# Kernel tuning notes

Measured on AMD Instinct MI355X. Metric: run time of the kernel, lower is better.

## Reference

```python
import jax, jax.numpy as jnp
import numpy as np

B, N, DIM, H = 16, 1024, 512, 8
HEAD_DIM = DIM // H
SCALE = HEAD_DIM ** -0.5


def _dct_matrix(m):
    # Orthonormal DCT-II matrix, matching cv2.dct: D[0,:]=sqrt(1/m),
    # D[k,n]=sqrt(2/m)*cos(pi*(2n+1)*k/(2m)) for k>0.
    n = jnp.arange(m, dtype=jnp.float32)
    k = n[:, None]
    D = jnp.sqrt(2.0 / m) * jnp.cos(jnp.pi * (2.0 * n[None, :] + 1.0) * k / (2.0 * m))
    return D.at[0, :].set(jnp.sqrt(1.0 / m))


def setup_inputs() -> dict:
    key = jax.random.key(0)
    ks = jax.random.split(key, 9)
    def lin(k, fan_in, shape):
        return jax.random.normal(k, shape, jnp.float32) * (1.0 / np.sqrt(fan_in))
    return {
        "x": jax.random.normal(ks[0], (B, N, DIM), jnp.float32),
        "qkv_w": lin(ks[1], DIM, (DIM, 3 * DIM)),
        "qkv_b": lin(ks[2], DIM, (3 * DIM,)),
        "proj_w": lin(ks[3], DIM, (DIM, DIM)),
        "proj_b": lin(ks[4], DIM, (DIM,)),
        "h1_w": lin(ks[5], DIM, (DIM, DIM // 4)),
        "h1_b": jnp.zeros((DIM // 4,), jnp.float32),
        "h2_w": lin(ks[6], DIM // 4, (DIM // 4, H)),
        "h2_b": jnp.zeros((H,), jnp.float32),
        "freq_w": jnp.float32(0.5),
    }


def _extract_dct_features(x):
    # x: (B, N, C). Mirrors extract_dct_features incl. the .detach() in torch.
    B_, N_, _ = x.shape
    m = int(np.ceil(np.sqrt(N_)))  # static
    x_mean = x.mean(axis=-1)                                   # (B, N)
    A = jnp.pad(x_mean, ((0, 0), (0, m * m - N_))).reshape(B_, m, m)
    D = _dct_matrix(m)
    dct2 = jnp.einsum('km,bmn,ln->bkl', D, A, D)               # 2D DCT per sample
    dct_feat = dct2.reshape(B_, m * m)[:, :N_]
    dct_feat = jnp.clip(dct_feat, -10.0, 10.0)
    norm = jnp.linalg.norm(dct_feat, axis=1, keepdims=True) + 1e-5
    return jax.lax.stop_gradient(dct_feat / norm)              # (B, N)


def reference(x, qkv_w, qkv_b, proj_w, proj_b, h1_w, h1_b, h2_w, h2_b, freq_w):
    B_, N_, C = x.shape
    # QKV projection -> (3, B, H, N, head_dim)
    qkv = (x @ qkv_w + qkv_b).reshape(B_, N_, 3, H, C // H)
    qkv = jnp.transpose(qkv, (2, 0, 3, 1, 4))
    q, k, v = qkv[0] * SCALE, qkv[1], qkv[2]
    attn = jnp.einsum('bhnd,bhmd->bhnm', q, k)                 # (B, H, N, N)

    # Frequency-domain attention term
    dct_feat = _extract_dct_features(x)                        # (B, N)
    x_avg = x.mean(axis=1)                                     # (B, C)
    head_w = jax.nn.relu(x_avg @ h1_w + h1_b) @ h2_w + h2_b    # (B, H)
    weighted = dct_feat[:, None, :] * head_w[:, :, None]       # (B, H, N)
    freq_attn = jnp.einsum('bhn,bhm->bnm', weighted, weighted) # (B, N, N)
    row_sum = jnp.maximum(freq_attn.sum(axis=-1, keepdims=True), 1e-5)
    freq_attn = jnp.clip(freq_attn / row_sum, 0.0, 1.0)

    aw = jax.nn.sigmoid(freq_w)
    attn = (1.0 - aw) * attn + aw * freq_attn[:, None, :, :]
    attn = jax.nn.softmax(attn, axis=-1)

    out = jnp.einsum('bhnm,bhmd->bhnd', attn, v)
    out = jnp.transpose(out, (0, 2, 1, 3)).reshape(B_, N_, C)
    return out @ proj_w + proj_b
```

## Files before the change

kernel.cpp:

```cpp
#include <hip/hip_runtime.h>
#include <hip/hip_bf16.h>
#include <math.h>

#define PI_F  3.14159265358979323846f
#define LOG2E 1.44269504088896340736f

typedef __attribute__((ext_vector_type(8))) short          bf16x8;
typedef __attribute__((ext_vector_type(8))) unsigned short ushort8;
typedef __attribute__((ext_vector_type(4))) float          f32x4;

__device__ __forceinline__ unsigned short f2bf(float f) {
  union { float f; unsigned u; } v; v.f = f;
  unsigned r = v.u + 0x7fffu + ((v.u >> 16) & 1u);
  return (unsigned short)(r >> 16);
}

__device__ __forceinline__ unsigned short f2bf_hw(float f) {
  __hip_bfloat16 h = __float2bfloat16(f);
  return *reinterpret_cast<unsigned short*>(&h);
}

#define GLOAD16(g, l)                                                         \
  __builtin_amdgcn_global_load_lds(                                           \
      (const __attribute__((address_space(1))) void*)(g),                     \
      (__attribute__((address_space(3))) void*)(l), 16, 0, 0)

static const size_t OFF_XB  = 0;
static const size_t OFF_QB  = 16777216;
static const size_t OFF_KB  = 33554432;
static const size_t OFF_VT  = 67108864;
static const size_t OFF_AO  = 83886080;
static const size_t OFF_WT  = 100663296;
static const size_t OFF_PWT = 102236160;
static const size_t OFF_XM  = 102760448;
static const size_t OFF_XA  = 102825984;
static const size_t OFF_DF  = 102858752;
static const size_t OFF_TS  = 102924288;
static const size_t OFF_CR  = 102924352;

__global__ __launch_bounds__(256) void k_xmean_cvt(const float* __restrict__ x,
                                                   float* __restrict__ xmean,
                                                   unsigned short* __restrict__ xb) {
  int row  = blockIdx.x * 4 + (threadIdx.x >> 6);
  int lane = threadIdx.x & 63;
  const float* px = x + (size_t)row * 512 + lane * 8;
  float4 a = ((const float4*)px)[0];
  float4 b = ((const float4*)px)[1];
  ushort8 o;
  o[0] = f2bf(a.x); o[1] = f2bf(a.y); o[2] = f2bf(a.z); o[3] = f2bf(a.w);
  o[4] = f2bf(b.x); o[5] = f2bf(b.y); o[6] = f2bf(b.z); o[7] = f2bf(b.w);
  *(ushort8*)(xb + (size_t)row * 512 + lane * 8) = o;
  float s = a.x + a.y + a.z + a.w + b.x + b.y + b.z + b.w;
  for (int off = 32; off; off >>= 1) s += __shfl_down(s, off);
  if (lane == 0) xmean[row] = s * (1.f / 512.f);
}

__global__ __launch_bounds__(512) void k_xavg(const unsigned short* __restrict__ xb,
                                              float* __restrict__ xavg) {
  int b = blockIdx.x, chunk = blockIdx.y;
  int c = threadIdx.x;
  const unsigned short* px = xb + ((size_t)b * 1024 + (size_t)chunk * 64) * 512 + c;
  float s = 0.f;
#pragma unroll 8
  for (int n = 0; n < 64; ++n) {
    unsigned u = (unsigned)px[(size_t)n * 512] << 16;
    s += *reinterpret_cast<float*>(&u);
  }
  atomicAdd(&xavg[b * 512 + c], s);
}

__global__ __launch_bounds__(1024) void k_dct(const float* __restrict__ xmean,
                                              float* __restrict__ dfeat,
                                              float* __restrict__ tsum) {
  __shared__ float A[32][33], Dm[32][33], Tm[32][33];
  __shared__ float red[1024];
  __shared__ float nrm;
  int b = blockIdx.x, t = threadIdx.x;
  int kk = t >> 5, nn = t & 31;
  A[kk][nn] = xmean[b * 1024 + t];
  float dv = (kk == 0) ? sqrtf(1.f / 32.f)
                       : sqrtf(2.f / 32.f) * cosf(PI_F * (2.f * nn + 1.f) * (float)kk / 64.f);
  Dm[kk][nn] = dv;
  __syncthreads();
  float acc = 0.f;
  for (int m = 0; m < 32; ++m) acc += Dm[kk][m] * A[m][nn];
  Tm[kk][nn] = acc;
  __syncthreads();
  float acc2 = 0.f;
  for (int n = 0; n < 32; ++n) acc2 += Tm[kk][n] * Dm[nn][n];
  float val = fminf(fmaxf(acc2, -10.f), 10.f);
  red[t] = val * val;
  __syncthreads();
  for (int s = 512; s; s >>= 1) { if (t < s) red[t] += red[t + s]; __syncthreads(); }
  if (t == 0) nrm = sqrtf(red[0]) + 1e-5f;
  __syncthreads();
  float dn = val / nrm;
  dfeat[b * 1024 + t] = dn;
  red[t] = dn;
  __syncthreads();
  for (int s = 512; s; s >>= 1) { if (t < s) red[t] += red[t + s]; __syncthreads(); }
  if (t == 0) tsum[b] = red[0];
}

__global__ __launch_bounds__(128) void k_headw(const float* __restrict__ xavg,
                                               const float* __restrict__ h1w,
                                               const float* __restrict__ h1b,
                                               const float* __restrict__ h2w,
                                               const float* __restrict__ h2b,
                                               const float* __restrict__ dfeat,
                                               const float* __restrict__ tsum,
                                               const float* __restrict__ freqw,
                                               float* __restrict__ crow) {
  __shared__ float xa[512];
  __shared__ float h1s[128];
  __shared__ float hw[8];
  int b = blockIdx.x, t = threadIdx.x;
  for (int i = t; i < 512; i += 128) xa[i] = xavg[b * 512 + i] * (1.f / 1024.f);
  __syncthreads();
  float acc = h1b[t];
  for (int c = 0; c < 512; ++c) acc += xa[c] * h1w[c * 128 + t];
  h1s[t] = fmaxf(acc, 0.f);
  __syncthreads();
  if (t < 8) {
    float a2 = h2b[t];
    for (int j = 0; j < 128; ++j) a2 += h1s[j] * h2w[j * 8 + t];
    hw[t] = a2;
  }
  __syncthreads();
  float s = 0.f;
#pragma unroll
  for (int h = 0; h < 8; ++h) s += hw[h] * hw[h];
  float Tb = tsum[b];
  const float aw2 = (1.f / (1.f + __expf(-freqw[0]))) * LOG2E;
  for (int n = t; n < 1024; n += 128) {
    float dn = dfeat[b * 1024 + n];
    float p = s * dn;
    crow[b * 1024 + n] = aw2 * p / fmaxf(p * Tb, 1e-5f);
  }
}

__global__ __launch_bounds__(256) void k_wtrans(const float* __restrict__ w,
                                                unsigned short* __restrict__ wt,
                                                int Nw) {
  __shared__ unsigned short T[64 * 65];
  int n0 = blockIdx.x * 64, k0 = blockIdx.y * 64;
  int t = threadIdx.x;
  int r = t >> 2, c0 = (t & 3) * 16;
  const float* src = w + (size_t)(k0 + r) * Nw + n0 + c0;
#pragma unroll
  for (int q = 0; q < 4; ++q) {
    float4 v4 = *(const float4*)(src + q * 4);
    T[(c0 + q * 4 + 0) * 65 + r] = f2bf(v4.x);
    T[(c0 + q * 4 + 1) * 65 + r] = f2bf(v4.y);
    T[(c0 + q * 4 + 2) * 65 + r] = f2bf(v4.z);
    T[(c0 + q * 4 + 3) * 65 + r] = f2bf(v4.w);
  }
  __syncthreads();
  int nl = t >> 2, koff = (t & 3) * 16;
  ushort8 o0, o1;
#pragma unroll
  for (int e = 0; e < 8; ++e) o0[e] = T[nl * 65 + koff + e];
#pragma unroll
  for (int e = 0; e < 8; ++e) o1[e] = T[nl * 65 + koff + 8 + e];
  unsigned short* dst = wt + (size_t)(n0 + nl) * 512 + k0 + koff;
  *(ushort8*)(dst) = o0;
  *(ushort8*)(dst + 8) = o1;
}

template <int MODE>
__global__ __launch_bounds__(256) void k_gemm(const unsigned short* __restrict__ A,
                                              const unsigned short* __restrict__ Bt,
                                              const float* __restrict__ bias,
                                              const float* __restrict__ freqw,
                                              unsigned short* __restrict__ o_q,
                                              unsigned short* __restrict__ o_k,
                                              unsigned short* __restrict__ o_vt,
                                              float* __restrict__ o_f) {
  __shared__ __align__(16) unsigned short As[128 * 64];
  __shared__ __align__(16) unsigned short Bs[128 * 64];
  const int t = threadIdx.x, w = t >> 6, l = t & 63;
  const int lg = l >> 4, ln = l & 15;
  const int wm = w >> 1, wn = w & 1;
  constexpr int NX = (MODE == 0) ? 12 : 4;
  const int bid = blockIdx.x, xcd = bid & 7, idx = bid >> 3;
  const int bx = idx % NX, by = xcd * 16 + idx / NX;
  const int row0 = by * 128, col0 = bx * 128;

  f32x4 acc[4][4];
#pragma unroll
  for (int i = 0; i < 4; ++i)
#pragma unroll
    for (int j = 0; j < 4; ++j) acc[i][j] = (f32x4){0.f, 0.f, 0.f, 0.f};

  int aoff[4][2], boff[4][2];
#pragma unroll
  for (int mt = 0; mt < 4; ++mt)
#pragma unroll
    for (int ks = 0; ks < 2; ++ks) {
      int ra = wm * 64 + mt * 16 + ln;
      aoff[mt][ks] = ra * 64 + (((lg + ks * 4) ^ (ra & 7)) << 3);
      int rb = wn * 64 + mt * 16 + ln;
      boff[mt][ks] = rb * 64 + (((lg + ks * 4) ^ (rb & 7)) << 3);
    }

  for (int k0 = 0; k0 < 512; k0 += 64) {
#pragma unroll
    for (int j = 0; j < 4; ++j) {
      int g = (j * 4 + w) * 64 + l;
      int row = g >> 3, slot = g & 7;
      int ss = slot ^ (row & 7);
      GLOAD16(A + (size_t)(row0 + row) * 512 + k0 + ss * 8, As + (size_t)(j * 4 + w) * 512);
      GLOAD16(Bt + (size_t)(col0 + row) * 512 + k0 + ss * 8, Bs + (size_t)(j * 4 + w) * 512);
    }
    __syncthreads();
#pragma unroll
    for (int ks = 0; ks < 2; ++ks) {
      bf16x8 av[4], bv[4];
#pragma unroll
      for (int mt = 0; mt < 4; ++mt) av[mt] = *(const bf16x8*)(As + aoff[mt][ks]);
#pragma unroll
      for (int nt = 0; nt < 4; ++nt) bv[nt] = *(const bf16x8*)(Bs + boff[nt][ks]);
#pragma unroll
      for (int mt = 0; mt < 4; ++mt)
#pragma unroll
        for (int nt = 0; nt < 4; ++nt)
          acc[mt][nt] = __builtin_amdgcn_mfma_f32_16x16x32_bf16(av[mt], bv[nt], acc[mt][nt], 0, 0, 0);
    }
    __syncthreads();
  }

  if (MODE == 0) {
    const int sel = col0 >> 9;
    if (sel == 2) {
      unsigned short* T = (wn == 0) ? As : Bs;
#pragma unroll
      for (int nt = 0; nt < 4; ++nt) {
        int dcol = nt * 16 + ln;
        float bcol = bias[col0 + wn * 64 + dcol];
#pragma unroll
        for (int mt = 0; mt < 4; ++mt)
#pragma unroll
          for (int r = 0; r < 4; ++r) {
            int rowL = wm * 64 + mt * 16 + lg * 4 + r;
            int slot = (rowL >> 3) ^ (dcol & 7);
            T[dcol * 128 + slot * 8 + (rowL & 7)] = f2bf(acc[mt][nt][r] + bcol);
          }
      }
      __syncthreads();
      int b_ = row0 >> 10, n0 = row0 & 1023;
      int h0 = (col0 & 511) >> 6;
      int dcol = t >> 2, rseg = (t & 3) * 32;
#pragma unroll
      for (int half = 0; half < 2; ++half) {
        const unsigned short* S = half ? Bs : As;
        size_t plane = ((size_t)(b_ * 8 + h0 + half)) << 16;
        unsigned short* dst = o_vt + plane + (size_t)dcol * 1024 + n0 + rseg;
#pragma unroll
        for (int j = 0; j < 4; ++j) {
          int slot = ((rseg >> 3) + j) ^ (dcol & 7);
          *(ushort8*)(dst + j * 8) = *(const ushort8*)(S + dcol * 128 + slot * 8);
        }
      }
      return;
    }
    unsigned short* outp = (sel == 0) ? o_q : o_k;
    const float aw = 1.f / (1.f + __expf(-freqw[0]));
    const float scl = (sel == 0) ? 0.125f * (1.f - aw) * LOG2E : 1.f;
#pragma unroll
    for (int nt = 0; nt < 4; ++nt) {
      int colg = col0 + wn * 64 + nt * 16 + ln;
      float bcol = bias[colg];
      int h = (colg >> 6) & 7, d = colg & 63;
#pragma unroll
      for (int mt = 0; mt < 4; ++mt)
#pragma unroll
        for (int r = 0; r < 4; ++r) {
          int row = row0 + wm * 64 + mt * 16 + lg * 4 + r;
          int bidx = row >> 10, n = row & 1023;
          float val = (acc[mt][nt][r] + bcol) * scl;
          outp[(((size_t)(bidx * 8 + h)) << 16) + (n << 6) + d] = f2bf(val);
        }
    }
  } else {
#pragma unroll
    for (int nt = 0; nt < 4; ++nt) {
      int colg = col0 + wn * 64 + nt * 16 + ln;
      float bcol = bias[colg];
#pragma unroll
      for (int mt = 0; mt < 4; ++mt)
#pragma unroll
        for (int r = 0; r < 4; ++r) {
          int row = row0 + wm * 64 + mt * 16 + lg * 4 + r;
          o_f[(size_t)row * 512 + colg] = acc[mt][nt][r] + bcol;
        }
    }
  }
}

__global__ __launch_bounds__(256) void k_attn(const unsigned short* __restrict__ qb,
                                              const unsigned short* __restrict__ kb,
                                              const unsigned short* __restrict__ vtg,
                                              const float* __restrict__ crow,
                                              const float* __restrict__ dfeat,
                                              const float* __restrict__ freqw,
                                              unsigned short* __restrict__ ao) {
  __shared__ __align__(16) unsigned short Ks[64 * 64];
  __shared__ __align__(16) unsigned short Vs[64 * 64];
  __shared__ __align__(16) unsigned short Ps[4][32 * 64];
  __shared__ __align__(16) float Df[1024];
  const int bid = blockIdx.x, xcd = bid & 7, idx = bid >> 3;
  const int bh = xcd * 16 + (idx >> 3), qt = idx & 7;
  const int b = bh >> 3, h = bh & 7;
  const int t = threadIdx.x, w = t >> 6, l = t & 63;
  const int lg = l >> 4, ln = l & 15;
  const size_t base = ((size_t)(b * 8 + h)) << 16;
  const float aw2 = (1.f / (1.f + __expf(-freqw[0]))) * LOG2E;

  *(float4*)(&Df[t * 4]) = *(const float4*)(dfeat + b * 1024 + t * 4);

  const int qrow0 = qt * 128 + w * 32;
  bf16x8 qf[2][2];
#pragma unroll
  for (int mt = 0; mt < 2; ++mt)
#pragma unroll
    for (int ks = 0; ks < 2; ++ks)
      qf[mt][ks] = *(const bf16x8*)(qb + base + (size_t)(qrow0 + mt * 16 + ln) * 64 + lg * 8 + ks * 32);

  float cr2[2][4];
#pragma unroll
  for (int mt = 0; mt < 2; ++mt)
#pragma unroll
    for (int r = 0; r < 4; ++r)
      cr2[mt][r] = crow[b * 1024 + qrow0 + mt * 16 + lg * 4 + r];

  f32x4 accO[2][4];
#pragma unroll
  for (int mt = 0; mt < 2; ++mt)
#pragma unroll
    for (int dt = 0; dt < 4; ++dt) accO[mt][dt] = (f32x4){0.f, 0.f, 0.f, 0.f};
  float mrow[2][4], psum[2][4];
#pragma unroll
  for (int mt = 0; mt < 2; ++mt)
#pragma unroll
    for (int r = 0; r < 4; ++r) { mrow[mt][r] = -1e30f; psum[mt][r] = 0.f; }

  int rdoff[2];
#pragma unroll
  for (int ks = 0; ks < 2; ++ks) rdoff[ks] = ln * 64 + (((lg + ks * 4) ^ (ln & 7)) << 3);
  int pwoff[4][4];
#pragma unroll
  for (int nt = 0; nt < 4; ++nt)
#pragma unroll
    for (int r = 0; r < 4; ++r) {
      int prow = lg * 4 + r;
      pwoff[nt][r] = prow * 64 + ((((nt << 1) | (ln >> 3)) ^ (prow & 7)) << 3) + (ln & 7);
    }

  for (int kt = 0; kt < 16; ++kt) {
    __syncthreads();
#pragma unroll
    for (int j = 0; j < 2; ++j) {
      int g = (j * 4 + w) * 64 + l;
      int row = g >> 3, slot = g & 7;
      int ss = slot ^ (row & 7);
      GLOAD16(kb + base + (size_t)(kt * 64 + row) * 64 + ss * 8, Ks + (size_t)(j * 4 + w) * 512);
      GLOAD16(vtg + base + (size_t)row * 1024 + kt * 64 + ss * 8, Vs + (size_t)(j * 4 + w) * 512);
    }
    __syncthreads();

    float dmv[4];
#pragma unroll
    for (int nt = 0; nt < 4; ++nt) dmv[nt] = Df[kt * 64 + nt * 16 + ln];
    f32x4 s[2][4];
#pragma unroll
    for (int mt = 0; mt < 2; ++mt)
#pragma unroll
      for (int nt = 0; nt < 4; ++nt)
#pragma unroll
        for (int r = 0; r < 4; ++r)
          s[mt][nt][r] = __builtin_amdgcn_fmed3f(cr2[mt][r] * dmv[nt], 0.f, aw2);
#pragma unroll
    for (int nt = 0; nt < 4; ++nt) {
      bf16x8 kf0 = *(const bf16x8*)(Ks + nt * 1024 + rdoff[0]);
      bf16x8 kf1 = *(const bf16x8*)(Ks + nt * 1024 + rdoff[1]);
#pragma unroll
      for (int mt = 0; mt < 2; ++mt) {
        s[mt][nt] = __builtin_amdgcn_mfma_f32_16x16x32_bf16(qf[mt][0], kf0, s[mt][nt], 0, 0, 0);
        s[mt][nt] = __builtin_amdgcn_mfma_f32_16x16x32_bf16(qf[mt][1], kf1, s[mt][nt], 0, 0, 0);
      }
    }

    float lmax[2][4];
    bool viol = false;
#pragma unroll
    for (int mt = 0; mt < 2; ++mt)
#pragma unroll
      for (int r = 0; r < 4; ++r) {
        lmax[mt][r] = fmaxf(fmaxf(s[mt][0][r], s[mt][1][r]), fmaxf(s[mt][2][r], s[mt][3][r]));
        viol = viol || (lmax[mt][r] > mrow[mt][r] + 8.f);
      }
    if (__any(viol)) {
#pragma unroll
      for (int mt = 0; mt < 2; ++mt)
#pragma unroll
        for (int r = 0; r < 4; ++r) {
          float pmax = lmax[mt][r];
          pmax = fmaxf(pmax, __shfl_xor(pmax, 1));
          pmax = fmaxf(pmax, __shfl_xor(pmax, 2));
          pmax = fmaxf(pmax, __shfl_xor(pmax, 4));
          pmax = fmaxf(pmax, __shfl_xor(pmax, 8));
          float mnew = fmaxf(mrow[mt][r], pmax);
          float sc = __builtin_amdgcn_exp2f(mrow[mt][r] - mnew);
          psum[mt][r] *= sc;
          mrow[mt][r] = mnew;
#pragma unroll
          for (int dt = 0; dt < 4; ++dt) accO[mt][dt][r] *= sc;
        }
    }
#pragma unroll
    for (int mt = 0; mt < 2; ++mt)
#pragma unroll
      for (int r = 0; r < 4; ++r) {
        float p0 = __builtin_amdgcn_exp2f(s[mt][0][r] - mrow[mt][r]);
        float p1 = __builtin_amdgcn_exp2f(s[mt][1][r] - mrow[mt][r]);
        float p2 = __builtin_amdgcn_exp2f(s[mt][2][r] - mrow[mt][r]);
        float p3 = __builtin_amdgcn_exp2f(s[mt][3][r] - mrow[mt][r]);
        psum[mt][r] += (p0 + p1) + (p2 + p3);
        Ps[w][mt * 1024 + pwoff[0][r]] = f2bf_hw(p0);
        Ps[w][mt * 1024 + pwoff[1][r]] = f2bf_hw(p1);
        Ps[w][mt * 1024 + pwoff[2][r]] = f2bf_hw(p2);
        Ps[w][mt * 1024 + pwoff[3][r]] = f2bf_hw(p3);
      }

    bf16x8 pa[2][2];
#pragma unroll
    for (int mt = 0; mt < 2; ++mt)
#pragma unroll
      for (int ks = 0; ks < 2; ++ks)
        pa[mt][ks] = *(const bf16x8*)(Ps[w] + mt * 1024 + rdoff[ks]);
#pragma unroll
    for (int dt = 0; dt < 4; ++dt) {
      bf16x8 vf0 = *(const bf16x8*)(Vs + dt * 1024 + rdoff[0]);
      bf16x8 vf1 = *(const bf16x8*)(Vs + dt * 1024 + rdoff[1]);
#pragma unroll
      for (int mt = 0; mt < 2; ++mt) {
        accO[mt][dt] = __builtin_amdgcn_mfma_f32_16x16x32_bf16(pa[mt][0], vf0, accO[mt][dt], 0, 0, 0);
        accO[mt][dt] = __builtin_amdgcn_mfma_f32_16x16x32_bf16(pa[mt][1], vf1, accO[mt][dt], 0, 0, 0);
      }
    }
  }

#pragma unroll
  for (int mt = 0; mt < 2; ++mt)
#pragma unroll
    for (int r = 0; r < 4; ++r) {
      float lr = psum[mt][r];
      lr += __shfl_xor(lr, 1);
      lr += __shfl_xor(lr, 2);
      lr += __shfl_xor(lr, 4);
      lr += __shfl_xor(lr, 8);
      float inv = 1.f / lr;
      int n = qrow0 + mt * 16 + lg * 4 + r;
#pragma unroll
      for (int dt = 0; dt < 4; ++dt)
        ao[((size_t)(b * 1024 + n)) * 512 + h * 64 + dt * 16 + ln] = f2bf(accO[mt][dt][r] * inv);
    }
}

extern "C" void kernel_launch(void* const* d_in, const int* in_sizes, int n_in,
                              void* d_out, int out_size, void* d_ws, size_t ws_size,
                              hipStream_t stream) {
  const float* x      = (const float*)d_in[0];
  const float* qkv_w  = (const float*)d_in[1];
  const float* qkv_b  = (const float*)d_in[2];
  const float* proj_w = (const float*)d_in[3];
  const float* proj_b = (const float*)d_in[4];
  const float* h1_w   = (const float*)d_in[5];
  const float* h1_b   = (const float*)d_in[6];
  const float* h2_w   = (const float*)d_in[7];
  const float* h2_b   = (const float*)d_in[8];
  const float* freq_w = (const float*)d_in[9];

  char* ws = (char*)d_ws;
  unsigned short* xb  = (unsigned short*)(ws + OFF_XB);
  unsigned short* qbp = (unsigned short*)(ws + OFF_QB);
  unsigned short* kbp = (unsigned short*)(ws + OFF_KB);
  unsigned short* vtg = (unsigned short*)(ws + OFF_VT);
  unsigned short* ao  = (unsigned short*)(ws + OFF_AO);
  unsigned short* wt  = (unsigned short*)(ws + OFF_WT);
  unsigned short* pwt = (unsigned short*)(ws + OFF_PWT);
  float* xmean = (float*)(ws + OFF_XM);
  float* xavg  = (float*)(ws + OFF_XA);
  float* dfeat = (float*)(ws + OFF_DF);
  float* tsum  = (float*)(ws + OFF_TS);
  float* crow  = (float*)(ws + OFF_CR);
  float* out   = (float*)d_out;

  hipMemsetAsync(xavg, 0, 16 * 512 * sizeof(float), stream);

  k_xmean_cvt<<<dim3(4096), 256, 0, stream>>>(x, xmean, xb);
  k_xavg<<<dim3(16, 16), 512, 0, stream>>>(xb, xavg);
  k_dct<<<dim3(16), 1024, 0, stream>>>(xmean, dfeat, tsum);
  k_headw<<<dim3(16), 128, 0, stream>>>(xavg, h1_w, h1_b, h2_w, h2_b, dfeat, tsum, freq_w, crow);
  k_wtrans<<<dim3(24, 8), 256, 0, stream>>>(qkv_w, wt, 1536);
  k_wtrans<<<dim3(8, 8), 256, 0, stream>>>(proj_w, pwt, 512);
  k_gemm<0><<<dim3(12 * 128), 256, 0, stream>>>(xb, wt, qkv_b, freq_w, qbp, kbp, vtg, nullptr);
  k_attn<<<dim3(1024), 256, 0, stream>>>(qbp, kbp, vtg, crow, dfeat, freq_w, ao);
  k_gemm<1><<<dim3(4 * 128), 256, 0, stream>>>(ao, pwt, proj_b, freq_w, nullptr, nullptr, nullptr, out);
}
```

Baseline: 187.9 us.

## Switch attention to transposed 32x32x16 MFMA and keep P in registers

Rewrites the attention inner loop to compute S transposed (K as the A operand, Q as B) with 32x32x16 bf16 MFMA, so each lane owns one query row. The softmax probabilities are packed into bf16 pairs and exchanged across lane halves with shuffles to form the A operand of the PV MFMA directly, which removes the per-wave LDS P buffer and its write/read round trip. Row max and sum need fewer cross-lane reductions. The rescale and final normalisation now use per-element shuffles, and register pressure from 32-lane accumulators may rise.

```diff
diff --git a/kernel.cpp b/kernel.cpp
--- a/kernel.cpp
+++ b/kernel.cpp
@@ -5,9 +5,11 @@
 #define PI_F  3.14159265358979323846f
 #define LOG2E 1.44269504088896340736f
 
-typedef __attribute__((ext_vector_type(8))) short          bf16x8;
-typedef __attribute__((ext_vector_type(8))) unsigned short ushort8;
-typedef __attribute__((ext_vector_type(4))) float          f32x4;
+typedef __attribute__((ext_vector_type(8)))  short          bf16x8;
+typedef __attribute__((ext_vector_type(8)))  unsigned short ushort8;
+typedef __attribute__((ext_vector_type(4)))  float          f32x4;
+typedef __attribute__((ext_vector_type(16))) float          f32x16;
+typedef __attribute__((ext_vector_type(4)))  int            i32x4;
 
 __device__ __forceinline__ unsigned short f2bf(float f) {
   union { float f; unsigned u; } v; v.f = f;
@@ -15,9 +17,10 @@
   return (unsigned short)(r >> 16);
 }
 
-__device__ __forceinline__ unsigned short f2bf_hw(float f) {
-  __hip_bfloat16 h = __float2bfloat16(f);
-  return *reinterpret_cast<unsigned short*>(&h);
+__device__ __forceinline__ unsigned pack2bf(float lo, float hi) {
+  float2 fv; fv.x = lo; fv.y = hi;
+  __hip_bfloat162 h2 = __float22bfloat162_rn(fv);
+  return *reinterpret_cast<unsigned*>(&h2);
 }
 
 #define GLOAD16(g, l)                                                         \
@@ -306,55 +309,31 @@
                                               unsigned short* __restrict__ ao) {
   __shared__ __align__(16) unsigned short Ks[64 * 64];
   __shared__ __align__(16) unsigned short Vs[64 * 64];
-  __shared__ __align__(16) unsigned short Ps[4][32 * 64];
   __shared__ __align__(16) float Df[1024];
   const int bid = blockIdx.x, xcd = bid & 7, idx = bid >> 3;
   const int bh = xcd * 16 + (idx >> 3), qt = idx & 7;
   const int b = bh >> 3, h = bh & 7;
   const int t = threadIdx.x, w = t >> 6, l = t & 63;
-  const int lg = l >> 4, ln = l & 15;
+  const int ln = l & 31, hi = l >> 5;
   const size_t base = ((size_t)(b * 8 + h)) << 16;
   const float aw2 = (1.f / (1.f + __expf(-freqw[0]))) * LOG2E;
 
   *(float4*)(&Df[t * 4]) = *(const float4*)(dfeat + b * 1024 + t * 4);
 
-  const int qrow0 = qt * 128 + w * 32;
-  bf16x8 qf[2][2];
-#pragma unroll
-  for (int mt = 0; mt < 2; ++mt)
-#pragma unroll
-    for (int ks = 0; ks < 2; ++ks)
-      qf[mt][ks] = *(const bf16x8*)(qb + base + (size_t)(qrow0 + mt * 16 + ln) * 64 + lg * 8 + ks * 32);
-
-  float cr2[2][4];
-#pragma unroll
-  for (int mt = 0; mt < 2; ++mt)
-#pragma unroll
-    for (int r = 0; r < 4; ++r)
-      cr2[mt][r] = crow[b * 1024 + qrow0 + mt * 16 + lg * 4 + r];
-
-  f32x4 accO[2][4];
-#pragma unroll
-  for (int mt = 0; mt < 2; ++mt)
-#pragma unroll
-    for (int dt = 0; dt < 4; ++dt) accO[mt][dt] = (f32x4){0.f, 0.f, 0.f, 0.f};
-  float mrow[2][4], psum[2][4];
-#pragma unroll
-  for (int mt = 0; mt < 2; ++mt)
-#pragma unroll
-    for (int r = 0; r < 4; ++r) { mrow[mt][r] = -1e30f; psum[mt][r] = 0.f; }
-
-  int rdoff[2];
-#pragma unroll
-  for (int ks = 0; ks < 2; ++ks) rdoff[ks] = ln * 64 + (((lg + ks * 4) ^ (ln & 7)) << 3);
-  int pwoff[4][4];
-#pragma unroll
-  for (int nt = 0; nt < 4; ++nt)
-#pragma unroll
-    for (int r = 0; r < 4; ++r) {
-      int prow = lg * 4 + r;
-      pwoff[nt][r] = prow * 64 + ((((nt << 1) | (ln >> 3)) ^ (prow & 7)) << 3) + (ln & 7);
-    }
+  const int qrow = qt * 128 + w * 32 + ln;
+  bf16x8 qf[4];
+#pragma unroll
+  for (int ks = 0; ks < 4; ++ks)
+    qf[ks] = *(const bf16x8*)(qb + base + (size_t)qrow * 64 + ks * 16 + hi * 8);
+
+  const float cr = crow[b * 1024 + qrow];
+
+  f32x16 accO[2];
+#pragma unroll
+  for (int db = 0; db < 2; ++db)
+#pragma unroll
+    for (int r = 0; r < 16; ++r) accO[db][r] = 0.f;
+  float mrow = -1e30f, psum = 0.f;
 
   for (int kt = 0; kt < 16; ++kt) {
     __syncthreads();
@@ -368,103 +347,88 @@
     }
     __syncthreads();
 
-    float dmv[4];
-#pragma unroll
-    for (int nt = 0; nt < 4; ++nt) dmv[nt] = Df[kt * 64 + nt * 16 + ln];
-    f32x4 s[2][4];
-#pragma unroll
-    for (int mt = 0; mt < 2; ++mt)
-#pragma unroll
-      for (int nt = 0; nt < 4; ++nt)
-#pragma unroll
-        for (int r = 0; r < 4; ++r)
-          s[mt][nt][r] = __builtin_amdgcn_fmed3f(cr2[mt][r] * dmv[nt], 0.f, aw2);
-#pragma unroll
-    for (int nt = 0; nt < 4; ++nt) {
-      bf16x8 kf0 = *(const bf16x8*)(Ks + nt * 1024 + rdoff[0]);
-      bf16x8 kf1 = *(const bf16x8*)(Ks + nt * 1024 + rdoff[1]);
-#pragma unroll
-      for (int mt = 0; mt < 2; ++mt) {
-        s[mt][nt] = __builtin_amdgcn_mfma_f32_16x16x32_bf16(qf[mt][0], kf0, s[mt][nt], 0, 0, 0);
-        s[mt][nt] = __builtin_amdgcn_mfma_f32_16x16x32_bf16(qf[mt][1], kf1, s[mt][nt], 0, 0, 0);
-      }
-    }
-
-    float lmax[2][4];
-    bool viol = false;
-#pragma unroll
-    for (int mt = 0; mt < 2; ++mt)
-#pragma unroll
-      for (int r = 0; r < 4; ++r) {
-        lmax[mt][r] = fmaxf(fmaxf(s[mt][0][r], s[mt][1][r]), fmaxf(s[mt][2][r], s[mt][3][r]));
-        viol = viol || (lmax[mt][r] > mrow[mt][r] + 8.f);
-      }
-    if (__any(viol)) {
-#pragma unroll
-      for (int mt = 0; mt < 2; ++mt)
-#pragma unroll
-        for (int r = 0; r < 4; ++r) {
-          float pmax = lmax[mt][r];
-          pmax = fmaxf(pmax, __shfl_xor(pmax, 1));
-          pmax = fmaxf(pmax, __shfl_xor(pmax, 2));
-          pmax = fmaxf(pmax, __shfl_xor(pmax, 4));
-          pmax = fmaxf(pmax, __shfl_xor(pmax, 8));
-          float mnew = fmaxf(mrow[mt][r], pmax);
-          float sc = __builtin_amdgcn_exp2f(mrow[mt][r] - mnew);
-          psum[mt][r] *= sc;
-          mrow[mt][r] = mnew;
-#pragma unroll
-          for (int dt = 0; dt < 4; ++dt) accO[mt][dt][r] *= sc;
+#pragma unroll
+    for (int kbk = 0; kbk < 2; ++kbk) {
+      float4 df4[4];
+#pragma unroll
+      for (int g = 0; g < 4; ++g)
+        df4[g] = *(const float4*)(&Df[kt * 64 + kbk * 32 + g * 8 + hi * 4]);
+      f32x16 sT;
+#pragma unroll
+      for (int r = 0; r < 16; ++r)
+        sT[r] = __builtin_amdgcn_fmed3f(cr * df4[r >> 2][r & 3], 0.f, aw2);
+
+#pragma unroll
+      for (int ks = 0; ks < 4; ++ks) {
+        int row = kbk * 32 + ln;
+        bf16x8 kf = *(const bf16x8*)(Ks + row * 64 + (((2 * ks + hi) ^ (row & 7)) << 3));
+        sT = __builtin_amdgcn_mfma_f32_32x32x16_bf16(kf, qf[ks], sT, 0, 0, 0);
+      }
+
+      float m01 = fmaxf(fmaxf(sT[0], sT[1]), fmaxf(sT[2], sT[3]));
+      float m23 = fmaxf(fmaxf(sT[4], sT[5]), fmaxf(sT[6], sT[7]));
+      float m45 = fmaxf(fmaxf(sT[8], sT[9]), fmaxf(sT[10], sT[11]));
+      float m67 = fmaxf(fmaxf(sT[12], sT[13]), fmaxf(sT[14], sT[15]));
+      float lmax = fmaxf(fmaxf(m01, m23), fmaxf(m45, m67));
+      lmax = fmaxf(lmax, __shfl_xor(lmax, 32));
+      if (__any(lmax > mrow + 8.f)) {
+        float mnew = fmaxf(mrow, lmax);
+        float sc = __builtin_amdgcn_exp2f(mrow - mnew);
+        psum *= sc;
+        mrow = mnew;
+#pragma unroll
+        for (int r = 0; r < 16; ++r) {
+          float scr = __shfl(sc, (r & 3) + 8 * (r >> 2) + 4 * hi);
+          accO[0][r] *= scr;
+          accO[1][r] *= scr;
         }
-    }
-#pragma unroll
-    for (int mt = 0; mt < 2; ++mt)
-#pragma unroll
-      for (int r = 0; r < 4; ++r) {
-        float p0 = __builtin_amdgcn_exp2f(s[mt][0][r] - mrow[mt][r]);
-        float p1 = __builtin_amdgcn_exp2f(s[mt][1][r] - mrow[mt][r]);
-        float p2 = __builtin_amdgcn_exp2f(s[mt][2][r] - mrow[mt][r]);
-        float p3 = __builtin_amdgcn_exp2f(s[mt][3][r] - mrow[mt][r]);
-        psum[mt][r] += (p0 + p1) + (p2 + p3);
-        Ps[w][mt * 1024 + pwoff[0][r]] = f2bf_hw(p0);
-        Ps[w][mt * 1024 + pwoff[1][r]] = f2bf_hw(p1);
-        Ps[w][mt * 1024 + pwoff[2][r]] = f2bf_hw(p2);
-        Ps[w][mt * 1024 + pwoff[3][r]] = f2bf_hw(p3);
-      }
-
-    bf16x8 pa[2][2];
-#pragma unroll
-    for (int mt = 0; mt < 2; ++mt)
-#pragma unroll
-      for (int ks = 0; ks < 2; ++ks)
-        pa[mt][ks] = *(const bf16x8*)(Ps[w] + mt * 1024 + rdoff[ks]);
-#pragma unroll
-    for (int dt = 0; dt < 4; ++dt) {
-      bf16x8 vf0 = *(const bf16x8*)(Vs + dt * 1024 + rdoff[0]);
-      bf16x8 vf1 = *(const bf16x8*)(Vs + dt * 1024 + rdoff[1]);
-#pragma unroll
-      for (int mt = 0; mt < 2; ++mt) {
-        accO[mt][dt] = __builtin_amdgcn_mfma_f32_16x16x32_bf16(pa[mt][0], vf0, accO[mt][dt], 0, 0, 0);
-        accO[mt][dt] = __builtin_amdgcn_mfma_f32_16x16x32_bf16(pa[mt][1], vf1, accO[mt][dt], 0, 0, 0);
-      }
-    }
-  }
-
-#pragma unroll
-  for (int mt = 0; mt < 2; ++mt)
-#pragma unroll
-    for (int r = 0; r < 4; ++r) {
-      float lr = psum[mt][r];
-      lr += __shfl_xor(lr, 1);
-      lr += __shfl_xor(lr, 2);
-      lr += __shfl_xor(lr, 4);
-      lr += __shfl_xor(lr, 8);
-      float inv = 1.f / lr;
-      int n = qrow0 + mt * 16 + lg * 4 + r;
-#pragma unroll
-      for (int dt = 0; dt < 4; ++dt)
-        ao[((size_t)(b * 1024 + n)) * 512 + h * 64 + dt * 16 + ln] = f2bf(accO[mt][dt][r] * inv);
-    }
+      }
+      float ps = 0.f;
+#pragma unroll
+      for (int r = 0; r < 16; ++r) {
+        sT[r] = __builtin_amdgcn_exp2f(sT[r] - mrow);
+        ps += sT[r];
+      }
+      psum += ps;
+
+      unsigned W[8];
+#pragma unroll
+      for (int m = 0; m < 8; ++m) W[m] = pack2bf(sT[2 * m], sT[2 * m + 1]);
+#pragma unroll
+      for (int k2 = 0; k2 < 2; ++k2) {
+        int bs = 4 * k2;
+        unsigned s0 = __shfl_xor((int)W[bs + 0], 32);
+        unsigned s1 = __shfl_xor((int)W[bs + 1], 32);
+        unsigned s2 = __shfl_xor((int)W[bs + 2], 32);
+        unsigned s3 = __shfl_xor((int)W[bs + 3], 32);
+        i32x4 wi;
+        wi[0] = hi ? (int)s2 : (int)W[bs + 0];
+        wi[1] = hi ? (int)s3 : (int)W[bs + 1];
+        wi[2] = hi ? (int)W[bs + 2] : (int)s0;
+        wi[3] = hi ? (int)W[bs + 3] : (int)s1;
+        bf16x8 pa = __builtin_bit_cast(bf16x8, wi);
+        int slotk = 2 * (2 * kbk + k2) + hi;
+#pragma unroll
+        for (int db = 0; db < 2; ++db) {
+          int rowv = db * 32 + ln;
+          bf16x8 vf = *(const bf16x8*)(Vs + rowv * 64 + ((slotk ^ (rowv & 7)) << 3));
+          accO[db] = __builtin_amdgcn_mfma_f32_32x32x16_bf16(pa, vf, accO[db], 0, 0, 0);
+        }
+      }
+    }
+  }
+
+  float lr = psum + __shfl_xor(psum, 32);
+  float inv = 1.f / lr;
+#pragma unroll
+  for (int r = 0; r < 16; ++r) {
+    int qreg = (r & 3) + 8 * (r >> 2) + 4 * hi;
+    float invr = __shfl(inv, qreg);
+    int n = qt * 128 + w * 32 + qreg;
+#pragma unroll
+    for (int db = 0; db < 2; ++db)
+      ao[((size_t)(b * 1024 + n)) * 512 + h * 64 + db * 32 + ln] = f2bf(accO[db][r] * invr);
+  }
 }
 
 extern "C" void kernel_launch(void* const* d_in, const int* in_sizes, int n_in,
```

Measured after the change: 191.1 us. About the same (+1.7%).
